# Kernel tuning notes

Hardware: AMD Instinct MI355X
Metric: run time of the kernel (lower is better)

## Reference

```python
import jax, jax.numpy as jnp
import numpy as np

NEG_SLOPE = 0.2
N_NODES = 50000


def gat_conv(x, src, dst, W, a_src, a_dst, b, n_nodes):
    """One PyG-style GATConv layer (eval mode, self-loops already in src/dst).
    x: [N, F_in]; W: [F_in, H*C]; a_src/a_dst: [H, C]; b: [H*C] or [C].
    Returns per-node, per-head outputs [N, H, C].
    """
    H, C = a_src.shape
    h = (x @ W).reshape(-1, H, C)                      # [N, H, C]
    s_src = jnp.sum(h * a_src[None], axis=-1)          # [N, H]
    s_dst = jnp.sum(h * a_dst[None], axis=-1)          # [N, H]
    e = jax.nn.leaky_relu(s_src[src] + s_dst[dst], NEG_SLOPE)   # [E, H]
    # segment softmax over incoming edges of each destination node
    m = jax.ops.segment_max(e, dst, num_segments=n_nodes)       # [N, H]
    w = jnp.exp(e - m[dst])                                     # [E, H]
    denom = jax.ops.segment_sum(w, dst, num_segments=n_nodes)   # [N, H]
    alpha = w / denom[dst]                                      # [E, H]
    # weighted aggregation of source features
    out = jax.ops.segment_sum(alpha[:, :, None] * h[src], dst, num_segments=n_nodes)
    return out  # [N, H, C]


def setup_inputs() -> dict:
    key = jax.random.key(0)
    ks = jax.random.split(key, 12)
    N, F_in, Hid, H, F_out = N_NODES, 128, 64, 4, 128
    E = 800000
    x = jax.random.normal(ks[0], (N, F_in), dtype=jnp.float32)
    edge_index = jax.random.randint(ks[1], (2, E), 0, N, dtype=jnp.int64)
    sc = 0.1
    return {
        "x": x,
        "edge_index": edge_index,
        "W1": jax.random.normal(ks[2], (F_in, H * Hid), dtype=jnp.float32) * sc,
        "att_src1": jax.random.normal(ks[3], (H, Hid), dtype=jnp.float32) * sc,
        "att_dst1": jax.random.normal(ks[4], (H, Hid), dtype=jnp.float32) * sc,
        "b1": jnp.zeros((H * Hid,), dtype=jnp.float32),
        "W2": jax.random.normal(ks[5], (H * Hid, F_out), dtype=jnp.float32) * sc,
        "att_src2": jax.random.normal(ks[6], (1, F_out), dtype=jnp.float32) * sc,
        "att_dst2": jax.random.normal(ks[7], (1, F_out), dtype=jnp.float32) * sc,
        "b2": jnp.zeros((F_out,), dtype=jnp.float32),
    }


def reference(x, edge_index, W1, att_src1, att_dst1, b1, W2, att_src2, att_dst2, b2):
    N = x.shape[0]
    # PyG GATConv adds self-loops by default
    loops = jnp.arange(N, dtype=edge_index.dtype)
    src = jnp.concatenate([edge_index[0], loops])
    dst = jnp.concatenate([edge_index[1], loops])
    # layer 1: heads=4, concat -> [N, H*Hid], then ELU (dropout is identity in eval)
    h1 = gat_conv(x, src, dst, W1, att_src1, att_dst1, b1, N)    # [N, H, Hid]
    h1 = h1.reshape(N, -1) + b1
    h1 = jax.nn.elu(h1)
    # layer 2: heads=1, concat=False -> mean over the single head
    h2 = gat_conv(h1, src, dst, W2, att_src2, att_dst2, b2, N)   # [N, 1, F_out]
    out = h2[:, 0, :] + b2
    return out
```

## Files before the change

### kernel.cpp

```cpp
#include <hip/hip_runtime.h>
#include <cmath>

typedef __attribute__((ext_vector_type(8))) short bf16x8;
typedef __attribute__((ext_vector_type(4))) float f32x4;

static __device__ __forceinline__ unsigned short f2bf(float f) {
    unsigned u = __float_as_uint(f);
    unsigned r = (u + 0x7fffu + ((u >> 16) & 1u)) >> 16;
    return (unsigned short)r;
}
static __device__ __forceinline__ unsigned packbf(float a, float b) {
    return (unsigned)f2bf(a) | ((unsigned)f2bf(b) << 16);
}
static __device__ __forceinline__ float bflo(unsigned u) { return __uint_as_float(u << 16); }
static __device__ __forceinline__ float bfhi(unsigned u) { return __uint_as_float(u & 0xffff0000u); }

__global__ void prep_k(const float* __restrict__ W1, const float* __restrict__ W2,
                       const int* __restrict__ dst,
                       unsigned short* __restrict__ Wt1, unsigned short* __restrict__ Wt2,
                       int* __restrict__ deg, int NW1, int NW2, int E) {
    int i = blockIdx.x * blockDim.x + threadIdx.x;
    if (i < NW1) { int nn = i / 128, k = i % 128; Wt1[i] = f2bf(W1[(size_t)k * 256 + nn]); return; }
    i -= NW1;
    if (i < NW2) { int nn = i / 256, k = i % 256; Wt2[i] = f2bf(W2[(size_t)k * 128 + nn]); return; }
    i -= NW2;
    if (i < E) atomicAdd(&deg[dst[i]], 1);
}

#define SCAN_BLK 256
#define SCAN_ELEMS 2048

__global__ void scan1_k(const int* __restrict__ deg, int* __restrict__ rowstart,
                        int* __restrict__ bsums, int N) {
    __shared__ int sh[SCAN_BLK];
    int t = threadIdx.x;
    int base = blockIdx.x * SCAN_ELEMS + t * 8;
    int vals[8];
    int sum = 0;
#pragma unroll
    for (int i = 0; i < 8; ++i) {
        int idx = base + i;
        vals[i] = (idx < N) ? (deg[idx] + 1) : 0;
        sum += vals[i];
    }
    sh[t] = sum;
    __syncthreads();
    for (int off = 1; off < SCAN_BLK; off <<= 1) {
        int v = (t >= off) ? sh[t - off] : 0;
        __syncthreads();
        sh[t] += v;
        __syncthreads();
    }
    int run = sh[t] - sum;
    if (t == SCAN_BLK - 1) bsums[blockIdx.x] = sh[t];
#pragma unroll
    for (int i = 0; i < 8; ++i) {
        int idx = base + i;
        if (idx < N) rowstart[idx] = run;
        run += vals[i];
    }
}
__global__ void scan2_k(int* __restrict__ bsums, int nb) {
    int lane = threadIdx.x;
    int own = (lane < nb) ? bsums[lane] : 0;
    int v = own;
    for (int off = 1; off < 64; off <<= 1) {
        int t = __shfl_up(v, off, 64);
        if (lane >= off) v += t;
    }
    if (lane < nb) bsums[lane] = v - own;
}
__global__ void scan3_init_k(int* __restrict__ rowstart, const int* __restrict__ bsums,
                             int* __restrict__ adj, int* __restrict__ cursor, int N, int total) {
    int i = blockIdx.x * blockDim.x + threadIdx.x;
    if (i < N) {
        int r = rowstart[i] + bsums[i / SCAN_ELEMS];
        rowstart[i] = r;
        adj[r] = i;
        cursor[i] = r + 1;
    } else if (i == N) {
        rowstart[N] = total;
    }
}
__global__ void scatter_k(const int* __restrict__ src, const int* __restrict__ dst, int E,
                          int* __restrict__ cursor, int* __restrict__ adj) {
    int e = blockIdx.x * blockDim.x + threadIdx.x;
    if (e >= E) return;
    int pos = atomicAdd(&cursor[dst[e]], 1);
    adj[pos] = src[e];
}

template<int K, int NOUT, int H, int C, bool AF32>
__global__ __launch_bounds__(256) void gemm_score_k(const void* __restrict__ Abv,
                                                    const unsigned* __restrict__ Bt,
                                                    unsigned short* __restrict__ Yb,
                                                    const float* __restrict__ asrc,
                                                    const float* __restrict__ adst,
                                                    float* __restrict__ ssrc,
                                                    float* __restrict__ sdst, int N) {
    __shared__ unsigned short As[128 * 64];
    __shared__ unsigned short Bs[128 * 64];
    __shared__ float sred[2][2][128];
    int tid = threadIdx.x;
    int lane = tid & 63, wid = tid >> 6;
    int wm = wid >> 1, wc = wid & 1;
    int m0 = blockIdx.x * 128;
    int n0 = blockIdx.y * 128;

    f32x4 acc[4][4] = {};

    for (int k0 = 0; k0 < K; k0 += 64) {
#pragma unroll
        for (int p = 0; p < 4; ++p) {
            int gl = p * 256 + tid;
            int row = gl >> 3, g = gl & 7;
            int grow = m0 + row; if (grow >= N) grow = N - 1;
            uint4 v;
            if constexpr (AF32) {
                const float* xp = (const float*)Abv + (size_t)grow * K + k0 + g * 8;
                float4 f0 = *reinterpret_cast<const float4*>(xp);
                float4 f1 = *reinterpret_cast<const float4*>(xp + 4);
                v.x = packbf(f0.x, f0.y); v.y = packbf(f0.z, f0.w);
                v.z = packbf(f1.x, f1.y); v.w = packbf(f1.z, f1.w);
            } else {
                v = *reinterpret_cast<const uint4*>((const unsigned*)Abv + (size_t)grow * (K / 2) + k0 / 2 + g * 4);
            }
            *reinterpret_cast<uint4*>((char*)As + row * 128 + ((g ^ (row & 7)) << 4)) = v;
        }
#pragma unroll
        for (int p = 0; p < 4; ++p) {
            int gl = p * 256 + tid;
            int row = gl >> 3, g = gl & 7;
            uint4 v = *reinterpret_cast<const uint4*>(Bt + (size_t)(n0 + row) * (K / 2) + k0 / 2 + g * 4);
            *reinterpret_cast<uint4*>((char*)Bs + row * 128 + ((g ^ (row & 7)) << 4)) = v;
        }
        __syncthreads();

        bf16x8 bfrag[2][4];
#pragma unroll
        for (int kk = 0; kk < 2; ++kk)
#pragma unroll
            for (int no = 0; no < 4; ++no) {
                int row = wc * 64 + no * 16 + (lane & 15);
                int g = kk * 4 + (lane >> 4);
                bfrag[kk][no] = *reinterpret_cast<const bf16x8*>((char*)Bs + row * 128 + ((g ^ (row & 7)) << 4));
            }
#pragma unroll
        for (int mo = 0; mo < 4; ++mo) {
#pragma unroll
            for (int kk = 0; kk < 2; ++kk) {
                int row = wm * 64 + mo * 16 + (lane & 15);
                int g = kk * 4 + (lane >> 4);
                bf16x8 afrag = *reinterpret_cast<const bf16x8*>((char*)As + row * 128 + ((g ^ (row & 7)) << 4));
#pragma unroll
                for (int no = 0; no < 4; ++no)
                    acc[mo][no] = __builtin_amdgcn_mfma_f32_16x16x32_bf16(afrag, bfrag[kk][no], acc[mo][no], 0, 0, 0);
            }
        }
        __syncthreads();
    }

#pragma unroll
    for (int mo = 0; mo < 4; ++mo)
#pragma unroll
        for (int no = 0; no < 4; ++no) {
            int col = n0 + wc * 64 + no * 16 + (lane & 15);
            int rbase = m0 + wm * 64 + mo * 16 + (lane >> 4) * 4;
#pragma unroll
            for (int j = 0; j < 4; ++j) {
                int row = rbase + j;
                if (row < N) Yb[(size_t)row * NOUT + col] = f2bf(acc[mo][no][j]);
            }
        }

    float cs[4], cd[4];
#pragma unroll
    for (int no = 0; no < 4; ++no) {
        int c0 = n0 + wc * 64 + no * 16 + (lane & 15);
        cs[no] = asrc[c0]; cd[no] = adst[c0];
    }
#pragma unroll
    for (int mo = 0; mo < 4; ++mo) {
        float ps[4], pd[4];
#pragma unroll
        for (int j = 0; j < 4; ++j) {
            ps[j] = 0.f; pd[j] = 0.f;
#pragma unroll
            for (int no = 0; no < 4; ++no) {
                ps[j] += acc[mo][no][j] * cs[no];
                pd[j] += acc[mo][no][j] * cd[no];
            }
        }
#pragma unroll
        for (int off = 8; off; off >>= 1)
#pragma unroll
            for (int j = 0; j < 4; ++j) {
                ps[j] += __shfl_xor(ps[j], off, 64);
                pd[j] += __shfl_xor(pd[j], off, 64);
            }
        if ((lane & 15) == 0) {
            int rl = wm * 64 + mo * 16 + (lane >> 4) * 4;
            if constexpr (C <= 64) {
                int hh = (n0 >> 6) + wc;
#pragma unroll
                for (int j = 0; j < 4; ++j) {
                    int row = m0 + rl + j;
                    if (row < N) {
                        ssrc[(size_t)row * H + hh] = ps[j];
                        sdst[(size_t)row * H + hh] = pd[j];
                    }
                }
            } else {
#pragma unroll
                for (int j = 0; j < 4; ++j) {
                    sred[wc][0][rl + j] = ps[j];
                    sred[wc][1][rl + j] = pd[j];
                }
            }
        }
    }
    if constexpr (C > 64) {
        __syncthreads();
        if (tid < 128) {
            int grow = m0 + tid;
            if (grow < N) {
                ssrc[grow] = sred[0][0][tid] + sred[1][0][tid];
                sdst[grow] = sred[0][1][tid] + sred[1][1][tid];
            }
        }
    }
}

template<int H, int C, int GRP, bool ELU, bool OUT_BF16>
__global__ void node_agg_k(const int* __restrict__ rowstart, const int* __restrict__ adj,
                           const float* __restrict__ ssrc, const float* __restrict__ sdst,
                           const unsigned* __restrict__ hb, const float* __restrict__ bias,
                           void* __restrict__ outp, int N) {
    constexpr int HC = H * C;
    constexpr int ROW_U = HC / 2;
    constexpr int ULN = ROW_U / GRP;
    constexpr int FPLn = ULN * 2;
    constexpr int NG = 64 / GRP;
    constexpr int NGB = 4 * NG;
    int lane = threadIdx.x & 63;
    int w = threadIdx.x >> 6;
    int g = lane / GRP, ln = lane % GRP;
    int gid = w * NG + g;
    int n = blockIdx.x * NGB + gid;
    if (n >= N) return;

    __shared__ int   s_tab[NGB][64];
    __shared__ float a_tab[NGB][64 * H];

    int r0 = rowstart[n], r1 = rowstart[n + 1];
    int deg = r1 - r0;

    float sd[H];
#pragma unroll
    for (int h = 0; h < H; ++h) sd[h] = sdst[n * H + h];

    int hA = (ln * FPLn) / C;
    const unsigned* hbl = hb + ln * ULN;
    float acc[FPLn];
#pragma unroll
    for (int f = 0; f < FPLn; ++f) acc[f] = 0.f;
    float l[H];
#pragma unroll
    for (int h = 0; h < H; ++h) l[h] = 0.f;

    if (deg <= 64) {
        for (int base = 0; base < deg; base += GRP) {
            int idx = base + ln;
            bool on = idx < deg;
            int s = adj[r0 + (on ? idx : 0)];
            float v[H];
            if constexpr (H == 4) {
                float4 sv = reinterpret_cast<const float4*>(ssrc)[s];
                v[0] = sv.x; v[1] = sv.y; v[2] = sv.z; v[3] = sv.w;
            } else {
                v[0] = ssrc[s];
            }
#pragma unroll
            for (int h = 0; h < H; ++h) {
                float t = v[h] + sd[h];
                t = t > 0.f ? t : 0.2f * t;
                float av = on ? __expf(t) : 0.f;
                l[h] += av;
                if (on) a_tab[gid][idx * H + h] = av;
            }
            if (on) s_tab[gid][idx] = s;
        }
#pragma unroll
        for (int off = GRP / 2; off; off >>= 1)
#pragma unroll
            for (int h = 0; h < H; ++h) l[h] += __shfl_xor(l[h], off, 64);

        int j = 0;
        for (; j + 3 < deg; j += 4) {
            int s0 = s_tab[gid][j],     s1 = s_tab[gid][j + 1];
            int s2 = s_tab[gid][j + 2], s3 = s_tab[gid][j + 3];
            float a0 = a_tab[gid][j * H + hA],       a1 = a_tab[gid][(j + 1) * H + hA];
            float a2 = a_tab[gid][(j + 2) * H + hA], a3 = a_tab[gid][(j + 3) * H + hA];
            uint4 u0 = *reinterpret_cast<const uint4*>(hbl + (size_t)s0 * ROW_U);
            uint4 u1 = *reinterpret_cast<const uint4*>(hbl + (size_t)s1 * ROW_U);
            uint4 u2 = *reinterpret_cast<const uint4*>(hbl + (size_t)s2 * ROW_U);
            uint4 u3 = *reinterpret_cast<const uint4*>(hbl + (size_t)s3 * ROW_U);
            acc[0] += a0 * bflo(u0.x); acc[1] += a0 * bfhi(u0.x);
            acc[2] += a0 * bflo(u0.y); acc[3] += a0 * bfhi(u0.y);
            acc[4] += a0 * bflo(u0.z); acc[5] += a0 * bfhi(u0.z);
            acc[6] += a0 * bflo(u0.w); acc[7] += a0 * bfhi(u0.w);
            acc[0] += a1 * bflo(u1.x); acc[1] += a1 * bfhi(u1.x);
            acc[2] += a1 * bflo(u1.y); acc[3] += a1 * bfhi(u1.y);
            acc[4] += a1 * bflo(u1.z); acc[5] += a1 * bfhi(u1.z);
            acc[6] += a1 * bflo(u1.w); acc[7] += a1 * bfhi(u1.w);
            acc[0] += a2 * bflo(u2.x); acc[1] += a2 * bfhi(u2.x);
            acc[2] += a2 * bflo(u2.y); acc[3] += a2 * bfhi(u2.y);
            acc[4] += a2 * bflo(u2.z); acc[5] += a2 * bfhi(u2.z);
            acc[6] += a2 * bflo(u2.w); acc[7] += a2 * bfhi(u2.w);
            acc[0] += a3 * bflo(u3.x); acc[1] += a3 * bfhi(u3.x);
            acc[2] += a3 * bflo(u3.y); acc[3] += a3 * bfhi(u3.y);
            acc[4] += a3 * bflo(u3.z); acc[5] += a3 * bfhi(u3.z);
            acc[6] += a3 * bflo(u3.w); acc[7] += a3 * bfhi(u3.w);
        }
        for (; j < deg; ++j) {
            int sj = s_tab[gid][j];
            float al = a_tab[gid][j * H + hA];
            uint4 u = *reinterpret_cast<const uint4*>(hbl + (size_t)sj * ROW_U);
            acc[0] += al * bflo(u.x); acc[1] += al * bfhi(u.x);
            acc[2] += al * bflo(u.y); acc[3] += al * bfhi(u.y);
            acc[4] += al * bflo(u.z); acc[5] += al * bfhi(u.z);
            acc[6] += al * bflo(u.w); acc[7] += al * bfhi(u.w);
        }
    } else {
        for (int e = r0 + ln; e < r1; e += GRP) {
            int s = adj[e];
#pragma unroll
            for (int h = 0; h < H; ++h) {
                float t = ssrc[s * H + h] + sd[h];
                t = t > 0.f ? t : 0.2f * t;
                l[h] += __expf(t);
            }
        }
#pragma unroll
        for (int off = GRP / 2; off; off >>= 1)
#pragma unroll
            for (int h = 0; h < H; ++h) l[h] += __shfl_xor(l[h], off, 64);
        float sdh = sd[hA];
        for (int e = r0; e < r1; ++e) {
            int s = adj[e];
            float t = ssrc[s * H + hA] + sdh;
            t = t > 0.f ? t : 0.2f * t;
            float al = __expf(t);
            uint4 u = *reinterpret_cast<const uint4*>(hbl + (size_t)s * ROW_U);
            acc[0] += al * bflo(u.x); acc[1] += al * bfhi(u.x);
            acc[2] += al * bflo(u.y); acc[3] += al * bfhi(u.y);
            acc[4] += al * bflo(u.z); acc[5] += al * bfhi(u.z);
            acc[6] += al * bflo(u.w); acc[7] += al * bfhi(u.w);
        }
    }

    float invl = __builtin_amdgcn_rcpf(l[hA]);
#pragma unroll
    for (int f = 0; f < FPLn; ++f) {
        float v = acc[f] * invl + bias[ln * FPLn + f];
        if (ELU) v = v > 0.f ? v : (__expf(v) - 1.f);
        acc[f] = v;
    }
    if constexpr (OUT_BF16) {
        unsigned* op = (unsigned*)outp + (size_t)n * ROW_U + ln * ULN;
        uint4 u = {packbf(acc[0], acc[1]), packbf(acc[2], acc[3]),
                   packbf(acc[4], acc[5]), packbf(acc[6], acc[7])};
        *reinterpret_cast<uint4*>(op) = u;
    } else {
        float* op = (float*)outp + (size_t)n * HC + ln * FPLn;
        *reinterpret_cast<float4*>(op) = make_float4(acc[0], acc[1], acc[2], acc[3]);
        *reinterpret_cast<float4*>(op + 4) = make_float4(acc[4], acc[5], acc[6], acc[7]);
    }
}

extern "C" void kernel_launch(void* const* d_in, const int* in_sizes, int n_in,
                              void* d_out, int out_size, void* d_ws, size_t ws_size,
                              hipStream_t stream) {
    const float* x   = (const float*)d_in[0];
    const int*   ei  = (const int*)d_in[1];
    const float* W1  = (const float*)d_in[2];
    const float* as1 = (const float*)d_in[3];
    const float* ad1 = (const float*)d_in[4];
    const float* b1  = (const float*)d_in[5];
    const float* W2  = (const float*)d_in[6];
    const float* as2 = (const float*)d_in[7];
    const float* ad2 = (const float*)d_in[8];
    const float* b2  = (const float*)d_in[9];
    float* out = (float*)d_out;

    const int N  = in_sizes[0] / 128;
    const int E  = in_sizes[1] / 2;
    const int ET = E + N;
    const int* src = ei;
    const int* dst = ei + E;

    unsigned* ws = (unsigned*)d_ws;
    unsigned* h1b   = ws;
    unsigned* agg1b = h1b   + (size_t)N * 128;
    unsigned* h2b   = agg1b + (size_t)N * 128;
    unsigned* Wt1   = h2b   + (size_t)N * 64;
    unsigned* Wt2   = Wt1   + 16384;
    float*    ssrc1 = (float*)(Wt2 + 16384);
    float*    sdst1 = ssrc1 + (size_t)N * 4;
    float*    ssrc2 = sdst1 + (size_t)N * 4;
    float*    sdst2 = ssrc2 + N;
    int*      deg   = (int*)(sdst2 + N);
    int*      rowst = deg + N;
    int*      bsums = rowst + N + 1;
    int*      adj   = bsums + 64;

    const int B = 256;
    auto blocks = [](size_t n, int b) { return (int)((n + b - 1) / b); };
    const int nscan = (N + SCAN_ELEMS - 1) / SCAN_ELEMS;

    hipMemsetAsync(deg, 0, (size_t)N * 4, stream);
    {
        int NW1 = 128 * 256, NW2 = 256 * 128;
        size_t tot = (size_t)NW1 + NW2 + E;
        prep_k<<<blocks(tot, B), B, 0, stream>>>(W1, W2, dst, (unsigned short*)Wt1,
                                                 (unsigned short*)Wt2, deg, NW1, NW2, E);
    }

    scan1_k<<<nscan, SCAN_BLK, 0, stream>>>(deg, rowst, bsums, N);
    scan2_k<<<1, 64, 0, stream>>>(bsums, nscan);
    scan3_init_k<<<blocks(N + 1, B), B, 0, stream>>>(rowst, bsums, adj, deg, N, ET);
    scatter_k<<<blocks(E, B), B, 0, stream>>>(src, dst, E, deg, adj);

    {
        dim3 g((N + 127) / 128, 2);
        gemm_score_k<128, 256, 4, 64, true><<<g, 256, 0, stream>>>(
            x, (const unsigned*)Wt1, (unsigned short*)h1b, as1, ad1, ssrc1, sdst1, N);
    }
    node_agg_k<4, 64, 32, true, true><<<(N + 7) / 8, 256, 0, stream>>>(rowst, adj, ssrc1, sdst1, h1b, b1, agg1b, N);

    {
        dim3 g((N + 127) / 128, 1);
        gemm_score_k<256, 128, 1, 128, false><<<g, 256, 0, stream>>>(
            agg1b, (const unsigned*)Wt2, (unsigned short*)h2b, as2, ad2, ssrc2, sdst2, N);
    }
    node_agg_k<1, 128, 16, false, false><<<(N + 15) / 16, 256, 0, stream>>>(rowst, adj, ssrc2, sdst2, h2b, b2, out, N);
}
```

Baseline: 230.0 us.

## Fold scan2 into scan3 and fuse edge scatter with layer-1 GEMM launch

Removes the single-block scan2 kernel by having each scan3 block serially sum the preceding block totals into a shared prefix. Merges the edge-scatter kernel and the layer-1 GEMM+score kernel into one launch, with block-index ranges dispatching to either job, so the atomic scatter can overlap the GEMM. This cuts two kernel launches and their serialization gaps. The cost is a small serial loop in thread 0 of each scan3 block and some shared-memory overhead on the scatter blocks, which now reserve the GEMM tiles.

```diff
diff --git a/kernel.cpp b/kernel.cpp
--- a/kernel.cpp
+++ b/kernel.cpp
@@ -60,21 +60,20 @@
         run += vals[i];
     }
 }
-__global__ void scan2_k(int* __restrict__ bsums, int nb) {
-    int lane = threadIdx.x;
-    int own = (lane < nb) ? bsums[lane] : 0;
-    int v = own;
-    for (int off = 1; off < 64; off <<= 1) {
-        int t = __shfl_up(v, off, 64);
-        if (lane >= off) v += t;
-    }
-    if (lane < nb) bsums[lane] = v - own;
-}
+
 __global__ void scan3_init_k(int* __restrict__ rowstart, const int* __restrict__ bsums,
                              int* __restrict__ adj, int* __restrict__ cursor, int N, int total) {
+    __shared__ int spre;
     int i = blockIdx.x * blockDim.x + threadIdx.x;
+    if (threadIdx.x == 0) {
+        int c = (blockIdx.x * blockDim.x) / SCAN_ELEMS;
+        int p = 0;
+        for (int j = 0; j < c; ++j) p += bsums[j];
+        spre = p;
+    }
+    __syncthreads();
     if (i < N) {
-        int r = rowstart[i] + bsums[i / SCAN_ELEMS];
+        int r = rowstart[i] + spre;
         rowstart[i] = r;
         adj[r] = i;
         cursor[i] = r + 1;
@@ -82,30 +81,19 @@
         rowstart[N] = total;
     }
 }
-__global__ void scatter_k(const int* __restrict__ src, const int* __restrict__ dst, int E,
-                          int* __restrict__ cursor, int* __restrict__ adj) {
-    int e = blockIdx.x * blockDim.x + threadIdx.x;
-    if (e >= E) return;
-    int pos = atomicAdd(&cursor[dst[e]], 1);
-    adj[pos] = src[e];
-}
 
 template<int K, int NOUT, int H, int C, bool AF32>
-__global__ __launch_bounds__(256) void gemm_score_k(const void* __restrict__ Abv,
-                                                    const unsigned* __restrict__ Bt,
-                                                    unsigned short* __restrict__ Yb,
-                                                    const float* __restrict__ asrc,
-                                                    const float* __restrict__ adst,
-                                                    float* __restrict__ ssrc,
-                                                    float* __restrict__ sdst, int N) {
+static __device__ __forceinline__ void gemm_score_body(
+        int m0, int n0, const void* __restrict__ Abv, const unsigned* __restrict__ Bt,
+        unsigned short* __restrict__ Yb, const float* __restrict__ asrc,
+        const float* __restrict__ adst, float* __restrict__ ssrc,
+        float* __restrict__ sdst, int N) {
     __shared__ unsigned short As[128 * 64];
     __shared__ unsigned short Bs[128 * 64];
     __shared__ float sred[2][2][128];
     int tid = threadIdx.x;
     int lane = tid & 63, wid = tid >> 6;
     int wm = wid >> 1, wc = wid & 1;
-    int m0 = blockIdx.x * 128;
-    int n0 = blockIdx.y * 128;
 
     f32x4 acc[4][4] = {};
 
@@ -229,6 +217,40 @@
             }
         }
     }
+}
+
+__global__ __launch_bounds__(256) void gemm1_scatter_k(
+        const float* __restrict__ x, const unsigned* __restrict__ Bt,
+        unsigned short* __restrict__ Yb, const float* __restrict__ asrc,
+        const float* __restrict__ adst, float* __restrict__ ssrc,
+        float* __restrict__ sdst, int N,
+        const int* __restrict__ src, const int* __restrict__ dst, int E,
+        int* __restrict__ cursor, int* __restrict__ adj, int SB, int GX) {
+    int bid = blockIdx.x;
+    if (bid < SB) {
+        int e = bid * 256 + threadIdx.x;
+        if (e < E) {
+            int pos = atomicAdd(&cursor[dst[e]], 1);
+            adj[pos] = src[e];
+        }
+        return;
+    }
+    int g = bid - SB;
+    int m0 = (g % GX) * 128;
+    int n0 = (g / GX) * 128;
+    gemm_score_body<128, 256, 4, 64, true>(m0, n0, x, Bt, Yb, asrc, adst, ssrc, sdst, N);
+}
+
+template<int K, int NOUT, int H, int C, bool AF32>
+__global__ __launch_bounds__(256) void gemm_score_k(const void* __restrict__ Abv,
+                                                    const unsigned* __restrict__ Bt,
+                                                    unsigned short* __restrict__ Yb,
+                                                    const float* __restrict__ asrc,
+                                                    const float* __restrict__ adst,
+                                                    float* __restrict__ ssrc,
+                                                    float* __restrict__ sdst, int N) {
+    gemm_score_body<K, NOUT, H, C, AF32>(blockIdx.x * 128, blockIdx.y * 128,
+                                         Abv, Bt, Yb, asrc, adst, ssrc, sdst, N);
 }
 
 template<int H, int C, int GRP, bool ELU, bool OUT_BF16>
@@ -427,14 +449,15 @@
     }
 
     scan1_k<<<nscan, SCAN_BLK, 0, stream>>>(deg, rowst, bsums, N);
-    scan2_k<<<1, 64, 0, stream>>>(bsums, nscan);
     scan3_init_k<<<blocks(N + 1, B), B, 0, stream>>>(rowst, bsums, adj, deg, N, ET);
-    scatter_k<<<blocks(E, B), B, 0, stream>>>(src, dst, E, deg, adj);
 
     {
-        dim3 g((N + 127) / 128, 2);
-        gemm_score_k<128, 256, 4, 64, true><<<g, 256, 0, stream>>>(
-            x, (const unsigned*)Wt1, (unsigned short*)h1b, as1, ad1, ssrc1, sdst1, N);
+        int SB = (E + B - 1) / B;
+        int GX = (N + 127) / 128;
+        dim3 g(SB + GX * 2);
+        gemm1_scatter_k<<<g, 256, 0, stream>>>(
+            x, (const unsigned*)Wt1, (unsigned short*)h1b, as1, ad1, ssrc1, sdst1, N,
+            src, dst, E, deg, adj, SB, GX);
     }
     node_agg_k<4, 64, 32, true, true><<<(N + 7) / 8, 256, 0, stream>>>(rowst, adj, ssrc1, sdst1, h1b, b1, agg1b, N);
 
```

Result: slower. 237.9 us (+3.4%).

## Split aggregation into alpha precompute and feature-sliced gather kernels

Applied to the files above, without the earlier changes.

Each fused node aggregation kernel is replaced by two passes. The first computes per-edge unnormalized attention weights and inverse softmax sums into workspace. The second gathers source features with blocks assigned per feature slice, so consecutive blocks touch the same columns and improve cache locality on the random gathers. It also folds the block-sum scan into the init kernel, where each block serially sums the preceding partials, removing a launch. The cost is extra kernels and an extra write and read of the per-edge alpha arrays, and alpha and adj are re-read once per slice.

```diff
diff --git a/kernel.cpp b/kernel.cpp
--- a/kernel.cpp
+++ b/kernel.cpp
@@ -60,21 +60,20 @@
         run += vals[i];
     }
 }
-__global__ void scan2_k(int* __restrict__ bsums, int nb) {
-    int lane = threadIdx.x;
-    int own = (lane < nb) ? bsums[lane] : 0;
-    int v = own;
-    for (int off = 1; off < 64; off <<= 1) {
-        int t = __shfl_up(v, off, 64);
-        if (lane >= off) v += t;
-    }
-    if (lane < nb) bsums[lane] = v - own;
-}
+
 __global__ void scan3_init_k(int* __restrict__ rowstart, const int* __restrict__ bsums,
                              int* __restrict__ adj, int* __restrict__ cursor, int N, int total) {
+    __shared__ int spre;
     int i = blockIdx.x * blockDim.x + threadIdx.x;
+    if (threadIdx.x == 0) {
+        int c = (blockIdx.x * blockDim.x) / SCAN_ELEMS;
+        int p = 0;
+        for (int j = 0; j < c; ++j) p += bsums[j];
+        spre = p;
+    }
+    __syncthreads();
     if (i < N) {
-        int r = rowstart[i] + bsums[i / SCAN_ELEMS];
+        int r = rowstart[i] + spre;
         rowstart[i] = r;
         adj[r] = i;
         cursor[i] = r + 1;
@@ -82,6 +81,7 @@
         rowstart[N] = total;
     }
 }
+
 __global__ void scatter_k(const int* __restrict__ src, const int* __restrict__ dst, int E,
                           int* __restrict__ cursor, int* __restrict__ adj) {
     int e = blockIdx.x * blockDim.x + threadIdx.x;
@@ -231,148 +231,124 @@
     }
 }
 
-template<int H, int C, int GRP, bool ELU, bool OUT_BF16>
-__global__ void node_agg_k(const int* __restrict__ rowstart, const int* __restrict__ adj,
-                           const float* __restrict__ ssrc, const float* __restrict__ sdst,
-                           const unsigned* __restrict__ hb, const float* __restrict__ bias,
-                           void* __restrict__ outp, int N) {
-    constexpr int HC = H * C;
-    constexpr int ROW_U = HC / 2;
-    constexpr int ULN = ROW_U / GRP;
-    constexpr int FPLn = ULN * 2;
+template<int H, int GRP>
+__global__ void alpha_k(const int* __restrict__ rowstart, const int* __restrict__ adj,
+                        const float* __restrict__ ssrc, const float* __restrict__ sdst,
+                        float* __restrict__ alpha, float* __restrict__ linv, int N, int ET) {
     constexpr int NG = 64 / GRP;
-    constexpr int NGB = 4 * NG;
     int lane = threadIdx.x & 63;
     int w = threadIdx.x >> 6;
     int g = lane / GRP, ln = lane % GRP;
-    int gid = w * NG + g;
-    int n = blockIdx.x * NGB + gid;
+    int n = blockIdx.x * (4 * NG) + w * NG + g;
     if (n >= N) return;
-
-    __shared__ int   s_tab[NGB][64];
-    __shared__ float a_tab[NGB][64 * H];
-
     int r0 = rowstart[n], r1 = rowstart[n + 1];
     int deg = r1 - r0;
-
     float sd[H];
 #pragma unroll
     for (int h = 0; h < H; ++h) sd[h] = sdst[n * H + h];
-
-    int hA = (ln * FPLn) / C;
-    const unsigned* hbl = hb + ln * ULN;
-    float acc[FPLn];
-#pragma unroll
-    for (int f = 0; f < FPLn; ++f) acc[f] = 0.f;
     float l[H];
 #pragma unroll
     for (int h = 0; h < H; ++h) l[h] = 0.f;
 
-    if (deg <= 64) {
-        for (int base = 0; base < deg; base += GRP) {
-            int idx = base + ln;
-            bool on = idx < deg;
-            int s = adj[r0 + (on ? idx : 0)];
-            float v[H];
-            if constexpr (H == 4) {
-                float4 sv = reinterpret_cast<const float4*>(ssrc)[s];
-                v[0] = sv.x; v[1] = sv.y; v[2] = sv.z; v[3] = sv.w;
-            } else {
-                v[0] = ssrc[s];
-            }
-#pragma unroll
-            for (int h = 0; h < H; ++h) {
-                float t = v[h] + sd[h];
-                t = t > 0.f ? t : 0.2f * t;
-                float av = on ? __expf(t) : 0.f;
-                l[h] += av;
-                if (on) a_tab[gid][idx * H + h] = av;
-            }
-            if (on) s_tab[gid][idx] = s;
-        }
-#pragma unroll
-        for (int off = GRP / 2; off; off >>= 1)
-#pragma unroll
-            for (int h = 0; h < H; ++h) l[h] += __shfl_xor(l[h], off, 64);
-
-        int j = 0;
-        for (; j + 3 < deg; j += 4) {
-            int s0 = s_tab[gid][j],     s1 = s_tab[gid][j + 1];
-            int s2 = s_tab[gid][j + 2], s3 = s_tab[gid][j + 3];
-            float a0 = a_tab[gid][j * H + hA],       a1 = a_tab[gid][(j + 1) * H + hA];
-            float a2 = a_tab[gid][(j + 2) * H + hA], a3 = a_tab[gid][(j + 3) * H + hA];
-            uint4 u0 = *reinterpret_cast<const uint4*>(hbl + (size_t)s0 * ROW_U);
-            uint4 u1 = *reinterpret_cast<const uint4*>(hbl + (size_t)s1 * ROW_U);
-            uint4 u2 = *reinterpret_cast<const uint4*>(hbl + (size_t)s2 * ROW_U);
-            uint4 u3 = *reinterpret_cast<const uint4*>(hbl + (size_t)s3 * ROW_U);
-            acc[0] += a0 * bflo(u0.x); acc[1] += a0 * bfhi(u0.x);
-            acc[2] += a0 * bflo(u0.y); acc[3] += a0 * bfhi(u0.y);
-            acc[4] += a0 * bflo(u0.z); acc[5] += a0 * bfhi(u0.z);
-            acc[6] += a0 * bflo(u0.w); acc[7] += a0 * bfhi(u0.w);
-            acc[0] += a1 * bflo(u1.x); acc[1] += a1 * bfhi(u1.x);
-            acc[2] += a1 * bflo(u1.y); acc[3] += a1 * bfhi(u1.y);
-            acc[4] += a1 * bflo(u1.z); acc[5] += a1 * bfhi(u1.z);
-            acc[6] += a1 * bflo(u1.w); acc[7] += a1 * bfhi(u1.w);
-            acc[0] += a2 * bflo(u2.x); acc[1] += a2 * bfhi(u2.x);
-            acc[2] += a2 * bflo(u2.y); acc[3] += a2 * bfhi(u2.y);
-            acc[4] += a2 * bflo(u2.z); acc[5] += a2 * bfhi(u2.z);
-            acc[6] += a2 * bflo(u2.w); acc[7] += a2 * bfhi(u2.w);
-            acc[0] += a3 * bflo(u3.x); acc[1] += a3 * bfhi(u3.x);
-            acc[2] += a3 * bflo(u3.y); acc[3] += a3 * bfhi(u3.y);
-            acc[4] += a3 * bflo(u3.z); acc[5] += a3 * bfhi(u3.z);
-            acc[6] += a3 * bflo(u3.w); acc[7] += a3 * bfhi(u3.w);
-        }
-        for (; j < deg; ++j) {
-            int sj = s_tab[gid][j];
-            float al = a_tab[gid][j * H + hA];
-            uint4 u = *reinterpret_cast<const uint4*>(hbl + (size_t)sj * ROW_U);
-            acc[0] += al * bflo(u.x); acc[1] += al * bfhi(u.x);
-            acc[2] += al * bflo(u.y); acc[3] += al * bfhi(u.y);
-            acc[4] += al * bflo(u.z); acc[5] += al * bfhi(u.z);
-            acc[6] += al * bflo(u.w); acc[7] += al * bfhi(u.w);
-        }
-    } else {
-        for (int e = r0 + ln; e < r1; e += GRP) {
-            int s = adj[e];
-#pragma unroll
-            for (int h = 0; h < H; ++h) {
-                float t = ssrc[s * H + h] + sd[h];
-                t = t > 0.f ? t : 0.2f * t;
-                l[h] += __expf(t);
-            }
-        }
-#pragma unroll
-        for (int off = GRP / 2; off; off >>= 1)
-#pragma unroll
-            for (int h = 0; h < H; ++h) l[h] += __shfl_xor(l[h], off, 64);
-        float sdh = sd[hA];
-        for (int e = r0; e < r1; ++e) {
-            int s = adj[e];
-            float t = ssrc[s * H + hA] + sdh;
+    for (int base = 0; base < deg; base += GRP) {
+        int idx = base + ln;
+        bool on = idx < deg;
+        int e = r0 + (on ? idx : 0);
+        int s = adj[e];
+        float v[H];
+        if constexpr (H == 4) {
+            float4 sv = reinterpret_cast<const float4*>(ssrc)[s];
+            v[0] = sv.x; v[1] = sv.y; v[2] = sv.z; v[3] = sv.w;
+        } else {
+            v[0] = ssrc[s];
+        }
+#pragma unroll
+        for (int h = 0; h < H; ++h) {
+            float t = v[h] + sd[h];
             t = t > 0.f ? t : 0.2f * t;
-            float al = __expf(t);
-            uint4 u = *reinterpret_cast<const uint4*>(hbl + (size_t)s * ROW_U);
-            acc[0] += al * bflo(u.x); acc[1] += al * bfhi(u.x);
-            acc[2] += al * bflo(u.y); acc[3] += al * bfhi(u.y);
-            acc[4] += al * bflo(u.z); acc[5] += al * bfhi(u.z);
-            acc[6] += al * bflo(u.w); acc[7] += al * bfhi(u.w);
-        }
-    }
-
-    float invl = __builtin_amdgcn_rcpf(l[hA]);
-#pragma unroll
-    for (int f = 0; f < FPLn; ++f) {
-        float v = acc[f] * invl + bias[ln * FPLn + f];
+            float av = on ? __expf(t) : 0.f;
+            l[h] += av;
+            if (on) alpha[(size_t)h * ET + e] = av;
+        }
+    }
+#pragma unroll
+    for (int off = GRP / 2; off; off >>= 1)
+#pragma unroll
+        for (int h = 0; h < H; ++h) l[h] += __shfl_xor(l[h], off, 64);
+    if (ln == 0) {
+#pragma unroll
+        for (int h = 0; h < H; ++h) linv[(size_t)h * N + n] = __builtin_amdgcn_rcpf(l[h]);
+    }
+}
+
+template<int ROW_U, int NSL, int HC, int H, bool ELU, bool OUT_BF16>
+__global__ void slice_agg_k(const int* __restrict__ rowstart, const int* __restrict__ adj,
+                            const float* __restrict__ alpha, const float* __restrict__ linv,
+                            const unsigned* __restrict__ hb, const float* __restrict__ bias,
+                            void* __restrict__ outp, int N, int ET) {
+    constexpr int SUBS = 8 / NSL;
+    constexpr int SL_BF = HC / NSL;
+    constexpr int SL_U = SL_BF / 2;
+    int b = blockIdx.x;
+    int xs = b & 7;
+    int slice = xs % NSL;
+    int sub = xs / NSL;
+    int chunk = (b >> 3) * SUBS + sub;
+    int lane = threadIdx.x & 63;
+    int w = threadIdx.x >> 6;
+    int g = lane >> 2, ln = lane & 3;
+    int n = chunk * 64 + w * 16 + g;
+    if (n >= N) return;
+    int r0 = rowstart[n], r1 = rowstart[n + 1];
+
+    int hh = (slice * SL_BF) / (HC / H);
+    const float* al = alpha + (size_t)hh * ET;
+    const unsigned* hbl = hb + slice * SL_U + ln * 4;
+
+    float acc[8];
+#pragma unroll
+    for (int f = 0; f < 8; ++f) acc[f] = 0.f;
+
+    int e = r0;
+    for (; e + 1 < r1; e += 2) {
+        int s0 = adj[e], s1 = adj[e + 1];
+        float a0 = al[e], a1 = al[e + 1];
+        uint4 u0 = *reinterpret_cast<const uint4*>(hbl + (size_t)s0 * ROW_U);
+        uint4 u1 = *reinterpret_cast<const uint4*>(hbl + (size_t)s1 * ROW_U);
+        acc[0] += a0 * bflo(u0.x); acc[1] += a0 * bfhi(u0.x);
+        acc[2] += a0 * bflo(u0.y); acc[3] += a0 * bfhi(u0.y);
+        acc[4] += a0 * bflo(u0.z); acc[5] += a0 * bfhi(u0.z);
+        acc[6] += a0 * bflo(u0.w); acc[7] += a0 * bfhi(u0.w);
+        acc[0] += a1 * bflo(u1.x); acc[1] += a1 * bfhi(u1.x);
+        acc[2] += a1 * bflo(u1.y); acc[3] += a1 * bfhi(u1.y);
+        acc[4] += a1 * bflo(u1.z); acc[5] += a1 * bfhi(u1.z);
+        acc[6] += a1 * bflo(u1.w); acc[7] += a1 * bfhi(u1.w);
+    }
+    if (e < r1) {
+        int s0 = adj[e];
+        float a0 = al[e];
+        uint4 u0 = *reinterpret_cast<const uint4*>(hbl + (size_t)s0 * ROW_U);
+        acc[0] += a0 * bflo(u0.x); acc[1] += a0 * bfhi(u0.x);
+        acc[2] += a0 * bflo(u0.y); acc[3] += a0 * bfhi(u0.y);
+        acc[4] += a0 * bflo(u0.z); acc[5] += a0 * bfhi(u0.z);
+        acc[6] += a0 * bflo(u0.w); acc[7] += a0 * bfhi(u0.w);
+    }
+
+    float invl = linv[(size_t)hh * N + n];
+    int fb = slice * SL_BF + ln * 8;
+#pragma unroll
+    for (int f = 0; f < 8; ++f) {
+        float v = acc[f] * invl + bias[fb + f];
         if (ELU) v = v > 0.f ? v : (__expf(v) - 1.f);
         acc[f] = v;
     }
     if constexpr (OUT_BF16) {
-        unsigned* op = (unsigned*)outp + (size_t)n * ROW_U + ln * ULN;
+        unsigned* op = (unsigned*)outp + (size_t)n * ROW_U + slice * SL_U + ln * 4;
         uint4 u = {packbf(acc[0], acc[1]), packbf(acc[2], acc[3]),
                    packbf(acc[4], acc[5]), packbf(acc[6], acc[7])};
         *reinterpret_cast<uint4*>(op) = u;
     } else {
-        float* op = (float*)outp + (size_t)n * HC + ln * FPLn;
+        float* op = (float*)outp + (size_t)n * HC + fb;
         *reinterpret_cast<float4*>(op) = make_float4(acc[0], acc[1], acc[2], acc[3]);
         *reinterpret_cast<float4*>(op + 4) = make_float4(acc[4], acc[5], acc[6], acc[7]);
     }
@@ -409,7 +385,11 @@
     float*    sdst1 = ssrc1 + (size_t)N * 4;
     float*    ssrc2 = sdst1 + (size_t)N * 4;
     float*    sdst2 = ssrc2 + N;
-    int*      deg   = (int*)(sdst2 + N);
+    float*    alpha1 = sdst2 + N;
+    float*    linv1  = alpha1 + (size_t)4 * ET;
+    float*    alpha2 = linv1 + (size_t)4 * N;
+    float*    linv2  = alpha2 + ET;
+    int*      deg   = (int*)(linv2 + N);
     int*      rowst = deg + N;
     int*      bsums = rowst + N + 1;
     int*      adj   = bsums + 64;
@@ -427,7 +407,6 @@
     }
 
     scan1_k<<<nscan, SCAN_BLK, 0, stream>>>(deg, rowst, bsums, N);
-    scan2_k<<<1, 64, 0, stream>>>(bsums, nscan);
     scan3_init_k<<<blocks(N + 1, B), B, 0, stream>>>(rowst, bsums, adj, deg, N, ET);
     scatter_k<<<blocks(E, B), B, 0, stream>>>(src, dst, E, deg, adj);
 
@@ -436,12 +415,23 @@
         gemm_score_k<128, 256, 4, 64, true><<<g, 256, 0, stream>>>(
             x, (const unsigned*)Wt1, (unsigned short*)h1b, as1, ad1, ssrc1, sdst1, N);
     }
-    node_agg_k<4, 64, 32, true, true><<<(N + 7) / 8, 256, 0, stream>>>(rowst, adj, ssrc1, sdst1, h1b, b1, agg1b, N);
+    alpha_k<4, 16><<<(N + 15) / 16, 256, 0, stream>>>(rowst, adj, ssrc1, sdst1, alpha1, linv1, N, ET);
+    {
+        int chunks = (N + 63) / 64;
+        slice_agg_k<128, 8, 256, 4, true, true><<<chunks * 8, 256, 0, stream>>>(
+            rowst, adj, alpha1, linv1, h1b, b1, agg1b, N, ET);
+    }
 
     {
         dim3 g((N + 127) / 128, 1);
         gemm_score_k<256, 128, 1, 128, false><<<g, 256, 0, stream>>>(
             agg1b, (const unsigned*)Wt2, (unsigned short*)h2b, as2, ad2, ssrc2, sdst2, N);
     }
-    node_agg_k<1, 128, 16, false, false><<<(N + 15) / 16, 256, 0, stream>>>(rowst, adj, ssrc2, sdst2, h2b, b2, out, N);
-}
+    alpha_k<1, 16><<<(N + 15) / 16, 256, 0, stream>>>(rowst, adj, ssrc2, sdst2, alpha2, linv2, N, ET);
+    {
+        int chunks = (N + 63) / 64;
+        int pairs = (chunks + 1) / 2;
+        slice_agg_k<64, 4, 128, 1, false, false><<<pairs * 8, 256, 0, stream>>>(
+            rowst, adj, alpha2, linv2, h2b, b2, out, N, ET);
+    }
+}
```

New measurement: 329.2 us. 1.43x slower.
